# Kernel optimization log

Hardware: AMD Instinct MI355X
Metric: run time of the kernel (lower is better)

The kernel has to match this reference:

```python
import jax, jax.numpy as jnp
import numpy as np

N_NODES = 50000
N_EDGES = 800000
IN_DIM, HID_DIM, OUT_DIM = 128, 128, 64


def setup_inputs() -> dict:
    key = jax.random.key(0)
    ks = jax.random.split(key, 12)
    x = jax.random.normal(ks[0], (N_NODES, IN_DIM), dtype=jnp.float32)
    src = jax.random.randint(ks[1], (N_EDGES,), 0, N_NODES, dtype=jnp.int32)
    dst = jax.random.randint(ks[2], (N_EDGES,), 0, N_NODES, dtype=jnp.int32)
    def lin(k, fan_in, fan_out):
        s = 1.0 / np.sqrt(fan_in)
        kw, kb = jax.random.split(k)
        W = jax.random.uniform(kw, (fan_in, fan_out), jnp.float32, -s, s)
        b = jax.random.uniform(kb, (fan_out,), jnp.float32, -s, s)
        return W, b
    W1, b1 = lin(ks[3], IN_DIM, HID_DIM)
    W2, b2 = lin(ks[4], HID_DIM, HID_DIM)
    W3, b3 = lin(ks[5], HID_DIM, OUT_DIM)
    Wf, bf = lin(ks[6], OUT_DIM, 1)
    return {"x": x, "src": src, "dst": dst,
            "W1": W1, "b1": b1, "W2": W2, "b2": b2,
            "W3": W3, "b3": b3, "Wf": Wf, "bf": bf}


def reference(x, src, dst, W1, b1, W2, b2, W3, b3, Wf, bf):
    n = x.shape[0]
    # GCN symmetric norm with self-loops: deg = in-degree + 1 (self loop)
    ones = jnp.ones(src.shape[0], x.dtype)
    deg = jax.ops.segment_sum(ones, dst, num_segments=n) + 1.0
    dinv = jax.lax.rsqrt(deg)                       # [N]
    edge_norm = dinv[src] * dinv[dst]               # [E]
    self_norm = dinv * dinv                         # [N], self-loop weight

    def gcn(h, W, b):
        h = h @ W                                   # transform first (PyG order)
        agg = jax.ops.segment_sum(h[src] * edge_norm[:, None], dst, num_segments=n)
        agg = agg + h * self_norm[:, None]          # self-loop contribution
        return agg + b

    h = jax.nn.relu(gcn(x, W1, b1))
    h = jax.nn.relu(gcn(h, W2, b2))
    h = jax.nn.relu(gcn(h, W3, b3))
    return h @ Wf + bf                              # [N, 1] per-node scores
```

## Files before the change

kernel.cpp:

```cpp
#include <hip/hip_runtime.h>
#include <hip/hip_bf16.h>

typedef short bf16x8 __attribute__((ext_vector_type(8)));
typedef float f32x4 __attribute__((ext_vector_type(4)));
typedef _Float16 f16x2 __attribute__((ext_vector_type(2)));

static __device__ __forceinline__ unsigned short f2bf_rne(float f) {
    unsigned int u = __float_as_uint(f);
    u += 0x7fff + ((u >> 16) & 1);
    return (unsigned short)(u >> 16);
}
static __device__ __forceinline__ float bf2f(unsigned short h) {
    return __uint_as_float(((unsigned int)h) << 16);
}


__global__ __launch_bounds__(256) void k_count_deg(const int* __restrict__ dst, int* __restrict__ deg, int E) {
    int e = blockIdx.x * blockDim.x + threadIdx.x;
    if (e < E) atomicAdd(&deg[dst[e]], 1);
}

__global__ __launch_bounds__(256) void k_dinv(const int* __restrict__ deg, float* __restrict__ dinv, int N) {
    int i = blockIdx.x * blockDim.x + threadIdx.x;
    if (i < N) dinv[i] = rsqrtf((float)deg[i] + 1.0f);
}

__global__ __launch_bounds__(1024) void k_chunk_sums(const int* __restrict__ deg, int* __restrict__ partial, int N) {
    __shared__ int wsum[16];
    int t = threadIdx.x;
    int i = blockIdx.x * 1024 + t;
    int v = (i < N) ? deg[i] : 0;
    for (int off = 32; off > 0; off >>= 1) v += __shfl_down(v, off, 64);
    if ((t & 63) == 0) wsum[t >> 6] = v;
    __syncthreads();
    if (t == 0) {
        int s = 0;
        #pragma unroll
        for (int k = 0; k < 16; ++k) s += wsum[k];
        partial[blockIdx.x] = s;
    }
}

__global__ void k_scan_partials(int* partial, int NB) {
    if (threadIdx.x == 0 && blockIdx.x == 0) {
        int run = 0;
        for (int b = 0; b < NB; ++b) { int t = partial[b]; partial[b] = run; run += t; }
    }
}

__global__ __launch_bounds__(1024) void k_chunk_scan(const int* __restrict__ deg, const int* __restrict__ partial,
                             int* __restrict__ row_start, int N) {
    __shared__ int s[1024];
    int t = threadIdx.x;
    int i = blockIdx.x * 1024 + t;
    int v = (i < N) ? deg[i] : 0;
    s[t] = v;
    __syncthreads();
    for (int off = 1; off < 1024; off <<= 1) {
        int x = (t >= off) ? s[t - off] : 0;
        __syncthreads();
        s[t] += x;
        __syncthreads();
    }
    if (i <= N) row_start[i] = partial[blockIdx.x] + s[t] - v;
}

__global__ __launch_bounds__(256) void k_scatter(const int* __restrict__ src, const int* __restrict__ dst,
                          const int* __restrict__ row_start, int* __restrict__ fill,
                          const float* __restrict__ dinv,
                          int2* __restrict__ cv, int E) {
    int e = blockIdx.x * blockDim.x + threadIdx.x;
    if (e < E) {
        int d = dst[e];
        int s = src[e];
        int r = atomicAdd(&fill[d], 1);
        cv[row_start[d] + r] = make_int2(s, __float_as_int(dinv[s]));
    }
}


__global__ __launch_bounds__(256) void k_wprep(const float* __restrict__ W,
                                               unsigned short* __restrict__ hi,
                                               unsigned short* __restrict__ lo,
                                               int BN, int total) {
    int idx = blockIdx.x * blockDim.x + threadIdx.x;
    if (idx >= total) return;
    int k = idx / BN, n = idx % BN;
    float w = W[idx];
    unsigned short h = f2bf_rne(w);
    unsigned short l = f2bf_rne(w - bf2f(h));
    int CT = BN >> 4;
    int kc = k >> 5, quad = (k >> 3) & 3, j = k & 7;
    int ct = n >> 4, c = n & 15;
    int slot = (((kc * CT + ct) * 4 + quad) * 16 + c) * 8 + j;
    hi[slot] = h;
    lo[slot] = l;
}


template<int BN>
__global__ __launch_bounds__(256, 2) void k_gemm_mfma(const float* __restrict__ A,
                        const unsigned short* __restrict__ Whi, const unsigned short* __restrict__ Wlo,
                        _Float16* __restrict__ C, int N) {
    constexpr int CT = BN / 16;
    __shared__ unsigned short AhiS[4 * 64 * 8];
    __shared__ unsigned short AloS[4 * 64 * 8];
    const int tid = threadIdx.x;
    const int wave = tid >> 6;
    const int lane = tid & 63;
    const int quad = lane >> 4;
    const int c16 = lane & 15;
    const int row0 = blockIdx.x * 64;

    f32x4 acc[CT];
    #pragma unroll
    for (int t = 0; t < CT; ++t) acc[t] = (f32x4){0.f, 0.f, 0.f, 0.f};

    for (int kc = 0; kc < 4; ++kc) {
        #pragma unroll
        for (int r = 0; r < 2; ++r) {
            int f4 = tid + r * 256;
            int arow = f4 >> 3;
            int c4 = f4 & 7;
            int grow = row0 + arow;
            float4 v = make_float4(0.f, 0.f, 0.f, 0.f);
            if (grow < N) v = *(const float4*)&A[(size_t)grow * 128 + kc * 32 + c4 * 4];
            unsigned short h0 = f2bf_rne(v.x), h1 = f2bf_rne(v.y), h2 = f2bf_rne(v.z), h3 = f2bf_rne(v.w);
            ushort4 hv = make_ushort4(h0, h1, h2, h3);
            ushort4 lv = make_ushort4(f2bf_rne(v.x - bf2f(h0)), f2bf_rne(v.y - bf2f(h1)),
                                      f2bf_rne(v.z - bf2f(h2)), f2bf_rne(v.w - bf2f(h3)));
            int q = c4 >> 1;
            int joff = (c4 & 1) * 4;
            int base = (q * 64 + arow) * 8 + joff;
            *(ushort4*)&AhiS[base] = hv;
            *(ushort4*)&AloS[base] = lv;
        }
        __syncthreads();

        int abase = (quad * 64 + wave * 16 + c16) * 8;
        bf16x8 ahi = *(const bf16x8*)&AhiS[abase];
        bf16x8 alo = *(const bf16x8*)&AloS[abase];

        #pragma unroll
        for (int ct = 0; ct < CT; ++ct) {
            size_t bslot = ((size_t)(kc * CT + ct) * 64 + lane) * 8;
            bf16x8 bhi = *(const bf16x8*)&Whi[bslot];
            bf16x8 blo = *(const bf16x8*)&Wlo[bslot];
            acc[ct] = __builtin_amdgcn_mfma_f32_16x16x32_bf16(ahi, bhi, acc[ct], 0, 0, 0);
            acc[ct] = __builtin_amdgcn_mfma_f32_16x16x32_bf16(ahi, blo, acc[ct], 0, 0, 0);
            acc[ct] = __builtin_amdgcn_mfma_f32_16x16x32_bf16(alo, bhi, acc[ct], 0, 0, 0);
        }
        __syncthreads();
    }

    #pragma unroll
    for (int ct = 0; ct < CT; ++ct) {
        #pragma unroll
        for (int r = 0; r < 4; ++r) {
            int grow = row0 + wave * 16 + quad * 4 + r;
            if (grow < N) C[(size_t)grow * BN + ct * 16 + c16] = (_Float16)acc[ct][r];
        }
    }
}


__global__ __launch_bounds__(256) void k_agg128(const _Float16* __restrict__ t, float* __restrict__ outp,
                      const int* __restrict__ row_start, const int2* __restrict__ cv,
                      const float* __restrict__ dinv, const float* __restrict__ bias,
                      int N) {
    int gid = blockIdx.x * blockDim.x + threadIdx.x;
    int node = gid >> 6;
    int lane = gid & 63;
    if (node >= N) return;
    int p = row_start[node];
    int end = row_start[node + 1];
    const f16x2* tp = (const f16x2*)t;
    float2 acc[4];
    #pragma unroll
    for (int j = 0; j < 4; ++j) acc[j] = make_float2(0.f, 0.f);

    while (p < end) {
        int idx = p + lane;
        int2 h = (idx < end) ? cv[idx] : make_int2(0, 0);
        int cnt = min(end - p, 64);
        int rounds = (cnt + 15) >> 4;
        for (int r = 0; r < rounds; ++r) {
            int base = r * 16;
            int s[16]; float w[16];
            #pragma unroll
            for (int j = 0; j < 16; ++j) {
                s[j] = __builtin_amdgcn_readlane(h.x, base + j);
                w[j] = __int_as_float(__builtin_amdgcn_readlane(h.y, base + j));
            }
            f16x2 v[16];
            #pragma unroll
            for (int j = 0; j < 16; ++j) v[j] = tp[s[j] * 64 + lane];
            #pragma unroll
            for (int j = 0; j < 16; ++j) {
                acc[j & 3].x += w[j] * (float)v[j].x;
                acc[j & 3].y += w[j] * (float)v[j].y;
            }
        }
        p += 64;
    }
    float di = dinv[node];
    f16x2 sv = tp[node * 64 + lane];
    float2 bv = ((const float2*)bias)[lane];
    float sx = (acc[0].x + acc[1].x) + (acc[2].x + acc[3].x);
    float sy = (acc[0].y + acc[1].y) + (acc[2].y + acc[3].y);
    float2 r;
    r.x = fmaxf(di * sx + di * di * (float)sv.x + bv.x, 0.f);
    r.y = fmaxf(di * sy + di * di * (float)sv.y + bv.y, 0.f);
    ((float2*)outp)[node * 64 + lane] = r;
}

__global__ __launch_bounds__(256) void k_agg64_final(const _Float16* __restrict__ t, float* __restrict__ outp,
                      const int* __restrict__ row_start, const int2* __restrict__ cv,
                      const float* __restrict__ dinv, const float* __restrict__ bias,
                      const float* __restrict__ Wf, const float* __restrict__ bf,
                      int N) {
    int gid = blockIdx.x * blockDim.x + threadIdx.x;
    int node = gid >> 6;
    int lane = gid & 63;
    if (node >= N) return;
    int p = row_start[node];
    int end = row_start[node + 1];
    float acc[4] = {0.f, 0.f, 0.f, 0.f};

    while (p < end) {
        int idx = p + lane;
        int2 h = (idx < end) ? cv[idx] : make_int2(0, 0);
        int cnt = min(end - p, 64);
        int rounds = (cnt + 15) >> 4;
        for (int r = 0; r < rounds; ++r) {
            int base = r * 16;
            int s[16]; float w[16];
            #pragma unroll
            for (int j = 0; j < 16; ++j) {
                s[j] = __builtin_amdgcn_readlane(h.x, base + j);
                w[j] = __int_as_float(__builtin_amdgcn_readlane(h.y, base + j));
            }
            _Float16 v[16];
            #pragma unroll
            for (int j = 0; j < 16; ++j) v[j] = t[s[j] * 64 + lane];
            #pragma unroll
            for (int j = 0; j < 16; ++j) acc[j & 3] += w[j] * (float)v[j];
        }
        p += 64;
    }
    float di = dinv[node];
    float r = di * ((acc[0] + acc[1]) + (acc[2] + acc[3])) + di * di * (float)t[node * 64 + lane] + bias[lane];
    r = fmaxf(r, 0.f);
    float v = r * Wf[lane];
    for (int off = 32; off > 0; off >>= 1) v += __shfl_down(v, off, 64);
    if (lane == 0) outp[node] = v + bf[0];
}


extern "C" void kernel_launch(void* const* d_in, const int* in_sizes, int n_in,
                              void* d_out, int out_size, void* d_ws, size_t ws_size,
                              hipStream_t stream) {
    const float* x  = (const float*)d_in[0];
    const int*   src = (const int*)d_in[1];
    const int*   dst = (const int*)d_in[2];
    const float* W1 = (const float*)d_in[3];
    const float* b1 = (const float*)d_in[4];
    const float* W2 = (const float*)d_in[5];
    const float* b2 = (const float*)d_in[6];
    const float* W3 = (const float*)d_in[7];
    const float* b3 = (const float*)d_in[8];
    const float* Wf = (const float*)d_in[9];
    const float* bf = (const float*)d_in[10];
    float* out = (float*)d_out;

    const int N = 50000;
    const int E = 800000;

    char* ws = (char*)d_ws;
    size_t off = 0;
    auto alloc = [&](size_t bytes) -> void* {
        void* p = (void*)(ws + off);
        off += (bytes + 511) & ~((size_t)511);
        return p;
    };
    int*   deg       = (int*)alloc((size_t)N * 4);
    int*   fill      = (int*)alloc((size_t)N * 4);
    float* dinv      = (float*)alloc((size_t)N * 4);
    int*   row_start = (int*)alloc((size_t)(N + 1) * 4);
    int*   partial   = (int*)alloc(64 * 4);
    int2*  cv        = (int2*)alloc((size_t)E * 8);
    _Float16* bufT   = (_Float16*)alloc((size_t)N * 128 * 2);
    float* bufH      = (float*)alloc((size_t)N * 128 * 4);
    unsigned short* W1hi = (unsigned short*)alloc(128 * 128 * 2);
    unsigned short* W1lo = (unsigned short*)alloc(128 * 128 * 2);
    unsigned short* W2hi = (unsigned short*)alloc(128 * 128 * 2);
    unsigned short* W2lo = (unsigned short*)alloc(128 * 128 * 2);
    unsigned short* W3hi = (unsigned short*)alloc(128 * 64 * 2);
    unsigned short* W3lo = (unsigned short*)alloc(128 * 64 * 2);

    hipMemsetAsync(deg, 0, (char*)dinv - (char*)deg, stream);

    k_count_deg<<<(E + 255) / 256, 256, 0, stream>>>(dst, deg, E);
    k_dinv<<<(N + 255) / 256, 256, 0, stream>>>(deg, dinv, N);
    int NB = (N + 1023) / 1024;
    k_chunk_sums<<<NB, 1024, 0, stream>>>(deg, partial, N);
    k_scan_partials<<<1, 64, 0, stream>>>(partial, NB);
    k_chunk_scan<<<NB, 1024, 0, stream>>>(deg, partial, row_start, N);
    k_scatter<<<(E + 255) / 256, 256, 0, stream>>>(src, dst, row_start, fill, dinv, cv, E);

    k_wprep<<<(128 * 128 + 255) / 256, 256, 0, stream>>>(W1, W1hi, W1lo, 128, 128 * 128);
    k_wprep<<<(128 * 128 + 255) / 256, 256, 0, stream>>>(W2, W2hi, W2lo, 128, 128 * 128);
    k_wprep<<<(128 * 64 + 255) / 256, 256, 0, stream>>>(W3, W3hi, W3lo, 64, 128 * 64);

    int gemmGrid = (N + 63) / 64;
    int aggGrid = (N * 64 + 255) / 256;

    k_gemm_mfma<128><<<gemmGrid, 256, 0, stream>>>(x, W1hi, W1lo, bufT, N);
    k_agg128<<<aggGrid, 256, 0, stream>>>(bufT, bufH, row_start, cv, dinv, b1, N);
    k_gemm_mfma<128><<<gemmGrid, 256, 0, stream>>>(bufH, W2hi, W2lo, bufT, N);
    k_agg128<<<aggGrid, 256, 0, stream>>>(bufT, bufH, row_start, cv, dinv, b2, N);
    k_gemm_mfma<64><<<gemmGrid, 256, 0, stream>>>(bufH, W3hi, W3lo, bufT, N);
    k_agg64_final<<<aggGrid, 256, 0, stream>>>(bufT, out, row_start, cv, dinv, b3, Wf, bf, N);
}
```

Before: 323.6 us.

## Fuse CSR build and weight prep into one cooperative kernel

```diff
diff --git a/kernel.cpp b/kernel.cpp
--- a/kernel.cpp
+++ b/kernel.cpp
@@ -1,5 +1,8 @@
 #include <hip/hip_runtime.h>
 #include <hip/hip_bf16.h>
+#include <hip/hip_cooperative_groups.h>
+
+namespace cg = cooperative_groups;
 
 typedef short bf16x8 __attribute__((ext_vector_type(8)));
 typedef float f32x4 __attribute__((ext_vector_type(4)));
@@ -14,77 +17,8 @@
     return __uint_as_float(((unsigned int)h) << 16);
 }
 
-
-__global__ __launch_bounds__(256) void k_count_deg(const int* __restrict__ dst, int* __restrict__ deg, int E) {
-    int e = blockIdx.x * blockDim.x + threadIdx.x;
-    if (e < E) atomicAdd(&deg[dst[e]], 1);
-}
-
-__global__ __launch_bounds__(256) void k_dinv(const int* __restrict__ deg, float* __restrict__ dinv, int N) {
-    int i = blockIdx.x * blockDim.x + threadIdx.x;
-    if (i < N) dinv[i] = rsqrtf((float)deg[i] + 1.0f);
-}
-
-__global__ __launch_bounds__(1024) void k_chunk_sums(const int* __restrict__ deg, int* __restrict__ partial, int N) {
-    __shared__ int wsum[16];
-    int t = threadIdx.x;
-    int i = blockIdx.x * 1024 + t;
-    int v = (i < N) ? deg[i] : 0;
-    for (int off = 32; off > 0; off >>= 1) v += __shfl_down(v, off, 64);
-    if ((t & 63) == 0) wsum[t >> 6] = v;
-    __syncthreads();
-    if (t == 0) {
-        int s = 0;
-        #pragma unroll
-        for (int k = 0; k < 16; ++k) s += wsum[k];
-        partial[blockIdx.x] = s;
-    }
-}
-
-__global__ void k_scan_partials(int* partial, int NB) {
-    if (threadIdx.x == 0 && blockIdx.x == 0) {
-        int run = 0;
-        for (int b = 0; b < NB; ++b) { int t = partial[b]; partial[b] = run; run += t; }
-    }
-}
-
-__global__ __launch_bounds__(1024) void k_chunk_scan(const int* __restrict__ deg, const int* __restrict__ partial,
-                             int* __restrict__ row_start, int N) {
-    __shared__ int s[1024];
-    int t = threadIdx.x;
-    int i = blockIdx.x * 1024 + t;
-    int v = (i < N) ? deg[i] : 0;
-    s[t] = v;
-    __syncthreads();
-    for (int off = 1; off < 1024; off <<= 1) {
-        int x = (t >= off) ? s[t - off] : 0;
-        __syncthreads();
-        s[t] += x;
-        __syncthreads();
-    }
-    if (i <= N) row_start[i] = partial[blockIdx.x] + s[t] - v;
-}
-
-__global__ __launch_bounds__(256) void k_scatter(const int* __restrict__ src, const int* __restrict__ dst,
-                          const int* __restrict__ row_start, int* __restrict__ fill,
-                          const float* __restrict__ dinv,
-                          int2* __restrict__ cv, int E) {
-    int e = blockIdx.x * blockDim.x + threadIdx.x;
-    if (e < E) {
-        int d = dst[e];
-        int s = src[e];
-        int r = atomicAdd(&fill[d], 1);
-        cv[row_start[d] + r] = make_int2(s, __float_as_int(dinv[s]));
-    }
-}
-
-
-__global__ __launch_bounds__(256) void k_wprep(const float* __restrict__ W,
-                                               unsigned short* __restrict__ hi,
-                                               unsigned short* __restrict__ lo,
-                                               int BN, int total) {
-    int idx = blockIdx.x * blockDim.x + threadIdx.x;
-    if (idx >= total) return;
+static __device__ __forceinline__ void wsplit_one(const float* W, unsigned short* hi,
+                                                  unsigned short* lo, int BN, int idx) {
     int k = idx / BN, n = idx % BN;
     float w = W[idx];
     unsigned short h = f2bf_rne(w);
@@ -95,6 +29,90 @@
     int slot = (((kc * CT + ct) * 4 + quad) * 16 + c) * 8 + j;
     hi[slot] = h;
     lo[slot] = l;
+}
+
+
+__global__ __launch_bounds__(256) void k_prep(
+        const int* __restrict__ src, const int* __restrict__ dst,
+        const float* __restrict__ W1, const float* __restrict__ W2, const float* __restrict__ W3,
+        int* __restrict__ deg, int* __restrict__ fill, float* __restrict__ dinv,
+        int* __restrict__ row_start, int* __restrict__ partial, int2* __restrict__ cv,
+        unsigned short* __restrict__ W1hi, unsigned short* __restrict__ W1lo,
+        unsigned short* __restrict__ W2hi, unsigned short* __restrict__ W2lo,
+        unsigned short* __restrict__ W3hi, unsigned short* __restrict__ W3lo,
+        int N, int E) {
+    cg::grid_group grid = cg::this_grid();
+    const int tid = threadIdx.x;
+    const int gtid = blockIdx.x * 256 + tid;
+    const int GSZ = gridDim.x * 256;
+    const int CHUNK = (50000 + 255) / 256;
+
+    __shared__ int red[4];
+    __shared__ int sc[256];
+
+    for (int i = gtid; i < N; i += GSZ) { deg[i] = 0; fill[i] = 0; }
+    for (int idx = gtid; idx < 128 * 128; idx += GSZ) {
+        wsplit_one(W1, W1hi, W1lo, 128, idx);
+        wsplit_one(W2, W2hi, W2lo, 128, idx);
+    }
+    for (int idx = gtid; idx < 128 * 64; idx += GSZ)
+        wsplit_one(W3, W3hi, W3lo, 64, idx);
+    grid.sync();
+
+    for (int e = gtid; e < E; e += GSZ) atomicAdd(&deg[dst[e]], 1);
+    grid.sync();
+
+    const int base = blockIdx.x * CHUNK;
+    {
+        int v = 0;
+        int i = base + tid;
+        if (tid < CHUNK && i < N) {
+            int d = deg[i];
+            v = d;
+            dinv[i] = rsqrtf((float)d + 1.0f);
+        }
+        for (int off = 32; off > 0; off >>= 1) v += __shfl_down(v, off, 64);
+        if ((tid & 63) == 0) red[tid >> 6] = v;
+        __syncthreads();
+        if (tid == 0) partial[blockIdx.x] = red[0] + red[1] + red[2] + red[3];
+    }
+    grid.sync();
+
+    if (blockIdx.x == 0) {
+        int pv = partial[tid];
+        sc[tid] = pv;
+        __syncthreads();
+        for (int off = 1; off < 256; off <<= 1) {
+            int x = (tid >= off) ? sc[tid - off] : 0;
+            __syncthreads();
+            sc[tid] += x;
+            __syncthreads();
+        }
+        partial[tid] = sc[tid] - pv;
+    }
+    grid.sync();
+
+    {
+        int i = base + tid;
+        int d = (tid < CHUNK && i < N) ? deg[i] : 0;
+        sc[tid] = d;
+        __syncthreads();
+        for (int off = 1; off < 256; off <<= 1) {
+            int x = (tid >= off) ? sc[tid - off] : 0;
+            __syncthreads();
+            sc[tid] += x;
+            __syncthreads();
+        }
+        if (tid < CHUNK && i < N) row_start[i] = partial[blockIdx.x] + sc[tid] - d;
+        if (gtid == 0) row_start[N] = E;
+    }
+    grid.sync();
+
+    for (int e = gtid; e < E; e += GSZ) {
+        int d = dst[e], s = src[e];
+        int r = atomicAdd(&fill[d], 1);
+        cv[row_start[d] + r] = make_int2(s, __float_as_int(dinv[s]));
+    }
 }
 
 
@@ -287,7 +305,7 @@
     int*   fill      = (int*)alloc((size_t)N * 4);
     float* dinv      = (float*)alloc((size_t)N * 4);
     int*   row_start = (int*)alloc((size_t)(N + 1) * 4);
-    int*   partial   = (int*)alloc(64 * 4);
+    int*   partial   = (int*)alloc(256 * 4);
     int2*  cv        = (int2*)alloc((size_t)E * 8);
     _Float16* bufT   = (_Float16*)alloc((size_t)N * 128 * 2);
     float* bufH      = (float*)alloc((size_t)N * 128 * 4);
@@ -298,19 +316,17 @@
     unsigned short* W3hi = (unsigned short*)alloc(128 * 64 * 2);
     unsigned short* W3lo = (unsigned short*)alloc(128 * 64 * 2);
 
-    hipMemsetAsync(deg, 0, (char*)dinv - (char*)deg, stream);
-
-    k_count_deg<<<(E + 255) / 256, 256, 0, stream>>>(dst, deg, E);
-    k_dinv<<<(N + 255) / 256, 256, 0, stream>>>(deg, dinv, N);
-    int NB = (N + 1023) / 1024;
-    k_chunk_sums<<<NB, 1024, 0, stream>>>(deg, partial, N);
-    k_scan_partials<<<1, 64, 0, stream>>>(partial, NB);
-    k_chunk_scan<<<NB, 1024, 0, stream>>>(deg, partial, row_start, N);
-    k_scatter<<<(E + 255) / 256, 256, 0, stream>>>(src, dst, row_start, fill, dinv, cv, E);
-
-    k_wprep<<<(128 * 128 + 255) / 256, 256, 0, stream>>>(W1, W1hi, W1lo, 128, 128 * 128);
-    k_wprep<<<(128 * 128 + 255) / 256, 256, 0, stream>>>(W2, W2hi, W2lo, 128, 128 * 128);
-    k_wprep<<<(128 * 64 + 255) / 256, 256, 0, stream>>>(W3, W3hi, W3lo, 64, 128 * 64);
+    {
+        int Nv = N, Ev = E;
+        void* args[] = {
+            (void*)&src, (void*)&dst, (void*)&W1, (void*)&W2, (void*)&W3,
+            (void*)&deg, (void*)&fill, (void*)&dinv, (void*)&row_start,
+            (void*)&partial, (void*)&cv,
+            (void*)&W1hi, (void*)&W1lo, (void*)&W2hi, (void*)&W2lo,
+            (void*)&W3hi, (void*)&W3lo, (void*)&Nv, (void*)&Ev
+        };
+        hipLaunchCooperativeKernel((void*)k_prep, dim3(256), dim3(256), args, 0, stream);
+    }
 
     int gemmGrid = (N + 63) / 64;
     int aggGrid = (N * 64 + 255) / 256;
```

After: 454.8 us. +40.6%, slower.
